# Optimization experiments

Hardware: AMD Instinct MI355X
Metric: run time of the kernel (lower is better)

Reference implementation:

```python
import jax, jax.numpy as jnp
import numpy as np

N_HEAD = 16
ROPE_CACHE = 2500  # Rotary module caches tables of length 2500
NEG_INF = -1e30


def _rope_tables(head_dim):
    inv_freq = 1.0 / (10000.0 ** (jnp.arange(0, head_dim, 2, dtype=jnp.float32) / head_dim))
    t = jnp.arange(ROPE_CACHE, dtype=jnp.float32)
    freqs = t[:, None] * inv_freq[None, :]            # (2500, head_dim//2)
    emb = jnp.concatenate([freqs, freqs], axis=-1)    # (2500, head_dim)
    return jnp.cos(emb), jnp.sin(emb)


def _rotate_half(x):
    h = x.shape[-1] // 2
    return jnp.concatenate([-x[..., h:], x[..., :h]], axis=-1)


def setup_inputs() -> dict:
    key = jax.random.key(0)
    ks = jax.random.split(key, 8)
    B, S, D = 2, 2048, 1024
    H = N_HEAD
    hd = D // H
    return {
        "qx": jax.random.normal(ks[0], (B, S, D), jnp.float32),
        "kvx": jax.random.normal(ks[1], (B, S, D), jnp.float32),
        "k_cache": jnp.zeros((B, H, S, hd), jnp.float32),
        "v_cache": jnp.zeros((B, H, S, hd), jnp.float32),
        "Wq": jax.random.normal(ks[2], (D, D), jnp.float32) * 0.02,
        "bq": jnp.zeros((D,), jnp.float32),
        "Wk": jax.random.normal(ks[3], (D, D), jnp.float32) * 0.02,
        "Wv": jax.random.normal(ks[4], (D, D), jnp.float32) * 0.02,
        "bv": jnp.zeros((D,), jnp.float32),
        "Wo": jax.random.normal(ks[5], (D, D), jnp.float32) * 0.02,
        "bo": jnp.zeros((D,), jnp.float32),
        "q_positions": jnp.arange(S, dtype=jnp.int32),
        "kv_positions": jnp.arange(S, dtype=jnp.int32),
    }


def reference(qx, kvx, k_cache, v_cache, Wq, bq, Wk, Wv, bv, Wo, bo, q_positions, kv_positions):
    B, Sq, D = qx.shape
    H = N_HEAD
    hd = D // H
    Skv = kvx.shape[1]
    cos, sin = _rope_tables(hd)
    # sqrt_qk_scale = sqrt(1) = 1, folded out.

    def rope(x, pos):  # x: (B, S, H, hd)
        c = cos[pos][None, :, None, :]
        s = sin[pos][None, :, None, :]
        return x * c + _rotate_half(x) * s

    # projections (torch Linear: y = x @ W.T + b; key has no bias)
    q = (qx @ Wq.T + bq).reshape(B, Sq, H, hd)
    q = rope(q, q_positions).transpose(0, 2, 1, 3)            # (B,H,Sq,hd)
    k = (kvx @ Wk.T).reshape(B, Skv, H, hd)
    k = rope(k, kv_positions).transpose(0, 2, 1, 3)           # (B,H,Skv,hd)
    v = (kvx @ Wv.T + bv).reshape(B, Skv, H, hd).transpose(0, 2, 1, 3)

    # KV-cache scatter update: k_cache[:, :, kv_positions] = k
    k_cache = k_cache.at[:, :, kv_positions].set(k)
    v_cache = v_cache.at[:, :, kv_positions].set(v)
    Sc = k_cache.shape[2]

    # SDPA (causal), scaled by 1/sqrt(head_dim) as in F.scaled_dot_product_attention
    scores = jnp.einsum('bhqd,bhkd->bhqk', q, k_cache) / jnp.sqrt(jnp.float32(hd))
    causal = jnp.arange(Sq)[:, None] >= jnp.arange(Sc)[None, :]
    scores = jnp.where(causal[None, None], scores, NEG_INF)
    attn = jax.nn.softmax(scores, axis=-1)
    wv = jnp.einsum('bhqk,bhkd->bhqd', attn, v_cache)

    out = wv.transpose(0, 2, 1, 3).reshape(B, Sq, D) @ Wo.T + bo
    return out
```

## Files before the change

kernel.cpp:

```cpp
#include <hip/hip_runtime.h>
#include <cstdint>
#include <cstddef>

#define NH   16
#define SEQ  2048
#define DM   1024
#define HD   64
#define KDIM 1024
#define MROWS 4096
#define CH   2

using short8  = __attribute__((ext_vector_type(8))) short;
using short4v = __attribute__((ext_vector_type(4))) short;
using floatx4 = __attribute__((ext_vector_type(4))) float;

__device__ __forceinline__ short f2bf(float f) {
  unsigned int u = __float_as_uint(f);
  u += 0x7fffu + ((u >> 16) & 1u);
  return (short)(u >> 16);
}
__device__ __forceinline__ float bf2f(short s) {
  return __uint_as_float(((unsigned int)(unsigned short)s) << 16);
}
__device__ __forceinline__ unsigned int pktrunc(float lo, float hi) {
  return __builtin_amdgcn_perm(__float_as_uint(hi), __float_as_uint(lo),
                               0x07060302u);
}

__device__ __forceinline__ void async_ld16(const void* g, void* l) {
  __builtin_amdgcn_global_load_lds(
      (const __attribute__((address_space(1))) void*)g,
      (__attribute__((address_space(3))) void*)l, 16, 0, 0);
}

struct Cvt8 {
  const float* src[8];
  void* dst[8];
  int n[8];
  const int* pos[8];
};

__global__ void convert8(Cvt8 a) {
  const int which = blockIdx.y;
  const int stride = gridDim.x * blockDim.x;
  if (which < 6) {
    const float4* s = (const float4*)a.src[which];
    short4v* d = (short4v*)a.dst[which];
    const int n4 = a.n[which] >> 2;
    for (int i = blockIdx.x * blockDim.x + threadIdx.x; i < n4; i += stride) {
      float4 v = s[i];
      short4v o;
      o.x = f2bf(v.x); o.y = f2bf(v.y); o.z = f2bf(v.z); o.w = f2bf(v.w);
      d[i] = o;
    }
  } else {
    const int* pos = a.pos[which];
    float2* d = (float2*)a.dst[which];
    const int n = a.n[which];
    for (int i = blockIdx.x * blockDim.x + threadIdx.x; i < n; i += stride) {
      int s = i >> 5, d1 = i & 31;
      float fr = __powf(10000.f, -(float)d1 * (1.f / 32.f));
      float ang = (float)pos[s] * fr;
      float sn, cs;
      __sincosf(ang, &sn, &cs);
      d[i] = make_float2(cs, sn);
    }
  }
}

__device__ __forceinline__ void gemm_core(const short* __restrict__ A,
                                          const short* __restrict__ B,
                                          int row0, int col0,
                                          short* As, short* Bs,
                                          floatx4 (&acc)[4][4], int tid) {
  const int lane = tid & 63;
  const int w = tid >> 6;
  const int quad = lane >> 4;
  const int ln = lane & 15;
  const int wr = w >> 1, wc = w & 1;

#pragma unroll
  for (int i = 0; i < 4; ++i)
#pragma unroll
    for (int j = 0; j < 4; ++j) acc[i][j] = (floatx4){0.f, 0.f, 0.f, 0.f};

  for (int k0 = 0; k0 < KDIM; k0 += 64) {
    __syncthreads();
#pragma unroll
    for (int g = 0; g < 4; ++g) {
      int slot = g * 256 + tid;
      int kk = slot >> 9, rem = slot & 511;
      int row = rem >> 2, grp = rem & 3;
      int src = k0 + kk * 32 + grp * 8;
      async_ld16(A + (size_t)(row0 + row) * KDIM + src, As + slot * 8);
      async_ld16(B + (size_t)(col0 + row) * KDIM + src, Bs + slot * 8);
    }
    __syncthreads();

#pragma unroll
    for (int ks = 0; ks < 2; ++ks) {
      short8 af[4], bfr[4];
#pragma unroll
      for (int i = 0; i < 4; ++i)
        af[i] = *(const short8*)(As + ks * 4096 + (wr * 64 + i * 16 + ln) * 32 + quad * 8);
#pragma unroll
      for (int j = 0; j < 4; ++j)
        bfr[j] = *(const short8*)(Bs + ks * 4096 + (wc * 64 + j * 16 + ln) * 32 + quad * 8);
#pragma unroll
      for (int i = 0; i < 4; ++i)
#pragma unroll
        for (int j = 0; j < 4; ++j)
          acc[i][j] = __builtin_amdgcn_mfma_f32_16x16x32_bf16(af[i], bfr[j], acc[i][j], 0, 0, 0);
    }
  }
}

__global__ __launch_bounds__(256) void proj_gemm(
    const short* __restrict__ qxb, const short* __restrict__ kvxb,
    const short* __restrict__ Wqb, const short* __restrict__ Wkb,
    const short* __restrict__ Wvb,
    const float* __restrict__ bq, const float* __restrict__ bv,
    short* __restrict__ Qo, short* __restrict__ Ko, short* __restrict__ Vt,
    const float2* __restrict__ qtab, const float2* __restrict__ ktab) {
  __shared__ __align__(16) short As[128 * 64];
  __shared__ __align__(16) short Bs[128 * 64];

  const int tid = threadIdx.x;
  const int lane = tid & 63;
  const int w = tid >> 6;
  const int quad = lane >> 4;
  const int ln = lane & 15;
  const int wr = w >> 1, wc = w & 1;
  const int z = blockIdx.z;

  int row0, col0;
  const short *A, *B;
  if (z == 2) {
    A = Wvb; B = kvxb;
    row0 = blockIdx.x * 128;
    col0 = blockIdx.y * 128;
  } else {
    A = z ? kvxb : qxb;
    B = z ? Wkb : Wqb;
    row0 = blockIdx.y * 128;
    col0 = blockIdx.x * 128;
  }

  floatx4 acc[4][4];
  gemm_core(A, B, row0, col0, As, Bs, acc, tid);

  if (z == 2) {
#pragma unroll
    for (int i = 0; i < 4; ++i)
#pragma unroll
      for (int r = 0; r < 4; ++r) {
        int nr = row0 + wr * 64 + i * 16 + quad * 4 + r;
        int h = nr >> 6, d = nr & 63;
        float bb = bv[nr];
        size_t base = ((size_t)(h)*HD + d) * SEQ;
#pragma unroll
        for (int j = 0; j < 4; ++j) {
          int sc = col0 + wc * 64 + j * 16 + ln;
          int b = sc >> 11, s = sc & (SEQ - 1);
          Vt[((size_t)b * NH * HD) * SEQ + base + s] = f2bf(acc[i][j][r] + bb);
        }
      }
  } else {
    const int colbase = col0 + wc * 64;
    const float scale = (z == 0) ? 0.125f : 1.0f;
    const float* bias = (z == 0) ? bq : nullptr;
    const float2* tab = (z == 0) ? qtab : ktab;
    short* Out = (z == 0) ? Qo : Ko;
#pragma unroll
    for (int j = 0; j < 2; ++j) {
      int col1 = colbase + j * 16 + ln;
      float b1 = bias ? bias[col1] : 0.f;
      float b2 = bias ? bias[col1 + 32] : 0.f;
      int h = col1 >> 6;
      int d1 = col1 & 63;
#pragma unroll
      for (int i = 0; i < 4; ++i)
#pragma unroll
        for (int r = 0; r < 4; ++r) {
          int row = row0 + wr * 64 + i * 16 + quad * 4 + r;
          int b = row >> 11, s = row & (SEQ - 1);
          float2 cs_sn = tab[s * 32 + d1];
          float x1 = acc[i][j][r] + b1;
          float x2 = acc[i][j + 2][r] + b2;
          float o1 = (x1 * cs_sn.x - x2 * cs_sn.y) * scale;
          float o2 = (x2 * cs_sn.x + x1 * cs_sn.y) * scale;
          size_t basq = ((((size_t)b * NH + h) * SEQ) + s) * HD;
          Out[basq + d1] = f2bf(o1);
          Out[basq + d1 + 32] = f2bf(o2);
        }
    }
  }
}

__global__ __launch_bounds__(256) void out_gemm(
    const short* __restrict__ Ab, const short* __restrict__ Bb,
    const float* __restrict__ bias, float* __restrict__ out) {
  __shared__ __align__(16) short As[64 * 64];
  __shared__ __align__(16) short Bs[128 * 64];
  const int tid = threadIdx.x;
  const int lane = tid & 63;
  const int w = tid >> 6;
  const int quad = lane >> 4;
  const int ln = lane & 15;
  const int wr = w >> 1, wc = w & 1;
  const int row0 = (blockIdx.x >> 3) * 64;
  const int col0 = (blockIdx.x & 7) * 128;

  floatx4 acc[2][4];
#pragma unroll
  for (int i = 0; i < 2; ++i)
#pragma unroll
    for (int j = 0; j < 4; ++j) acc[i][j] = (floatx4){0.f, 0.f, 0.f, 0.f};

  for (int k0 = 0; k0 < KDIM; k0 += 64) {
    __syncthreads();
    {
#pragma unroll
      for (int g = 0; g < 2; ++g) {
        int slot = g * 256 + tid;
        int kk = slot >> 8, rem = slot & 255;
        int row = rem >> 2, grp = rem & 3;
        async_ld16(Ab + (size_t)(row0 + row) * KDIM + k0 + kk * 32 + grp * 8,
                   As + slot * 8);
      }
#pragma unroll
      for (int g = 0; g < 4; ++g) {
        int slot = g * 256 + tid;
        int kk = slot >> 9, rem = slot & 511;
        int row = rem >> 2, grp = rem & 3;
        async_ld16(Bb + (size_t)(col0 + row) * KDIM + k0 + kk * 32 + grp * 8,
                   Bs + slot * 8);
      }
    }
    __syncthreads();

#pragma unroll
    for (int ks = 0; ks < 2; ++ks) {
      short8 af[2], bfr[4];
#pragma unroll
      for (int i = 0; i < 2; ++i)
        af[i] = *(const short8*)(As + ks * 2048 + (wr * 32 + i * 16 + ln) * 32 + quad * 8);
#pragma unroll
      for (int j = 0; j < 4; ++j)
        bfr[j] = *(const short8*)(Bs + ks * 4096 + (wc * 64 + j * 16 + ln) * 32 + quad * 8);
#pragma unroll
      for (int i = 0; i < 2; ++i)
#pragma unroll
        for (int j = 0; j < 4; ++j)
          acc[i][j] = __builtin_amdgcn_mfma_f32_16x16x32_bf16(af[i], bfr[j], acc[i][j], 0, 0, 0);
    }
  }

#pragma unroll
  for (int j = 0; j < 4; ++j) {
    int col = col0 + wc * 64 + j * 16 + ln;
    float bb = bias[col];
#pragma unroll
    for (int i = 0; i < 2; ++i)
#pragma unroll
      for (int r = 0; r < 4; ++r) {
        int row = row0 + wr * 32 + i * 16 + quad * 4 + r;
        out[(size_t)row * DM + col] = acc[i][j][r] + bb;
      }
  }
}

__global__ __launch_bounds__(256) void attn_partial(
    const short* __restrict__ Q, const short* __restrict__ Kc,
    const short* __restrict__ Vtg, short* __restrict__ Po,
    float* __restrict__ Lo) {
  const int tid = threadIdx.x;
  const int lane = tid & 63;
  const int w = tid >> 6;
  const int quad = lane >> 4;
  const int ln = lane & 15;
  const int bh = blockIdx.y;
  const int bx = blockIdx.x;
  const int qt = 31 - (bx >> 1);
  const int ch = bx & (CH - 1);
  if (ch > qt) return;

  const int q0 = qt * 64;
  const int wlo = q0 + w * 16;

  const short* Qb = Q + (size_t)bh * SEQ * HD;
  const short* Kb = Kc + (size_t)bh * SEQ * HD;
  const short* Vb = Vtg + (size_t)bh * HD * SEQ;

  __shared__ __align__(16) short Ks[2 * 64 * 32];
  __shared__ __align__(16) short Vs[2 * 64 * 32];
  __shared__ __align__(16) short Pt[4][16 * 72];

  short8 qa[2];
#pragma unroll
  for (int kk = 0; kk < 2; ++kk)
    qa[kk] = *(const short8*)(Qb + (size_t)(wlo + ln) * HD + quad * 8 + kk * 32);

  floatx4 oacc[4];
  float lp = 0.f;
#pragma unroll
  for (int jd = 0; jd < 4; ++jd) oacc[jd] = (floatx4){0.f, 0.f, 0.f, 0.f};

  for (int t = ch * 64; t <= q0; t += CH * 64) {
    __syncthreads();
#pragma unroll
    for (int g = 0; g < 2; ++g) {
      int slot = (w * 2 + g) * 64 + lane;
      int kk = slot >> 8, rowi = (slot >> 2) & 63, grp = slot & 3;
      async_ld16(Kb + (size_t)(t + rowi) * HD + kk * 32 + grp * 8,
                 (char*)Ks + slot * 16);
      async_ld16(Vb + (size_t)rowi * SEQ + t + kk * 32 + grp * 8,
                 (char*)Vs + slot * 16);
    }
    __syncthreads();

    floatx4 sacc[4];
#pragma unroll
    for (int c = 0; c < 4; ++c) sacc[c] = (floatx4){0.f, 0.f, 0.f, 0.f};
#pragma unroll
    for (int kk = 0; kk < 2; ++kk)
#pragma unroll
      for (int c = 0; c < 4; ++c) {
        short8 kb = *(const short8*)(Ks + kk * 2048 + (c * 16 + ln) * 32 + quad * 8);
        sacc[c] = __builtin_amdgcn_mfma_f32_16x16x32_bf16(kb, qa[kk], sacc[c], 0, 0, 0);
      }

    const bool dmask = (t == q0);
#pragma unroll
    for (int c = 0; c < 4; ++c) {
      float p[4];
#pragma unroll
      for (int r = 0; r < 4; ++r) {
        float pv = __expf(sacc[c][r]);
        if (dmask) {
          int sp = t + c * 16 + quad * 4 + r;
          int qq = wlo + ln;
          if (sp > qq) pv = 0.f;
        }
        lp += pv;
        p[r] = pv;
      }
      uint2 uu;
      uu.x = pktrunc(p[0], p[1]);
      uu.y = pktrunc(p[2], p[3]);
      *(uint2*)(&Pt[w][ln * 72 + c * 16 + quad * 4]) = uu;
    }

#pragma unroll
    for (int kk = 0; kk < 2; ++kk) {
      short8 pb = *(const short8*)(&Pt[w][ln * 72 + kk * 32 + quad * 8]);
#pragma unroll
      for (int jd = 0; jd < 4; ++jd) {
        short8 va = *(const short8*)(Vs + kk * 2048 + (jd * 16 + ln) * 32 + quad * 8);
        oacc[jd] = __builtin_amdgcn_mfma_f32_16x16x32_bf16(va, pb, oacc[jd], 0, 0, 0);
      }
    }
  }

  const size_t idx = ((size_t)bh * 32 + qt) * CH + ch;
  short* Pob = Po + idx * 4096;
#pragma unroll
  for (int jd = 0; jd < 4; ++jd) {
    short4v pk;
#pragma unroll
    for (int r = 0; r < 4; ++r) pk[r] = f2bf(oacc[jd][r]);
    *(short4v*)(Pob + (w * 16 + ln) * 64 + jd * 16 + quad * 4) = pk;
  }
  float l = lp;
  l += __shfl_xor(l, 16, 64);
  l += __shfl_xor(l, 32, 64);
  if (quad == 0) Lo[idx * 64 + w * 16 + ln] = l;
}

__global__ __launch_bounds__(256) void attn_reduce(
    const short* __restrict__ Po, const float* __restrict__ Lo,
    short* __restrict__ Ov) {
  const int qt = blockIdx.x;
  const int bh = blockIdx.y;
  const int b = bh >> 4, h = bh & 15;
  const int tid = threadIdx.x;
  const int ql = tid >> 2;
  const int d0 = (tid & 3) * 16;
  const int nch = (qt >= 1) ? CH : 1;
  const size_t i0 = ((size_t)bh * 32 + qt) * CH;

  float l = Lo[i0 * 64 + ql];
  const short8* p0 = (const short8*)(Po + i0 * 4096 + ql * 64 + d0);
  short8 a0 = p0[0], a1 = p0[1];
  float acc[16];
#pragma unroll
  for (int e = 0; e < 8; ++e) { acc[e] = bf2f(a0[e]); acc[8 + e] = bf2f(a1[e]); }
  if (nch == 2) {
    l += Lo[(i0 + 1) * 64 + ql];
    const short8* p1 = (const short8*)(Po + (i0 + 1) * 4096 + ql * 64 + d0);
    short8 c0 = p1[0], c1 = p1[1];
#pragma unroll
    for (int e = 0; e < 8; ++e) { acc[e] += bf2f(c0[e]); acc[8 + e] += bf2f(c1[e]); }
  }
  float inv = 1.f / l;
  short8 o0, o1;
#pragma unroll
  for (int e = 0; e < 8; ++e) { o0[e] = f2bf(acc[e] * inv); o1[e] = f2bf(acc[8 + e] * inv); }
  int s = qt * 64 + ql;
  short* dst = Ov + ((size_t)b * SEQ + s) * DM + h * HD + d0;
  *(short8*)dst = o0;
  *((short8*)dst + 1) = o1;
}

extern "C" void kernel_launch(void* const* d_in, const int* in_sizes, int n_in,
                              void* d_out, int out_size, void* d_ws, size_t ws_size,
                              hipStream_t stream) {
  const float* qx  = (const float*)d_in[0];
  const float* kvx = (const float*)d_in[1];
  const float* Wq = (const float*)d_in[4];
  const float* bq = (const float*)d_in[5];
  const float* Wk = (const float*)d_in[6];
  const float* Wv = (const float*)d_in[7];
  const float* bv = (const float*)d_in[8];
  const float* Wo = (const float*)d_in[9];
  const float* bo = (const float*)d_in[10];
  const int* qpos  = (const int*)d_in[11];
  const int* kvpos = (const int*)d_in[12];

  char* ws = (char*)d_ws;
  short* qxb  = (short*)(ws + 0);
  short* kvxb = (short*)(ws + 8388608);
  short* Wqb  = (short*)(ws + 16777216);
  short* Wkb  = (short*)(ws + 18874368);
  short* Wvb  = (short*)(ws + 20971520);
  short* Wob  = (short*)(ws + 23068672);
  short* Qbf  = (short*)(ws + 25165824);
  short* Kbf  = (short*)(ws + 33554432);
  short* Vtb  = (short*)(ws + 41943040);
  short* WVbf = (short*)(ws + 50331648);
  float2* qtab = (float2*)(ws + 50331648);
  float2* ktab = (float2*)(ws + 50331648 + 524288);
  short* Po = (short*)(ws + 0);
  float* Lo = (float*)(ws + 16777216);

  Cvt8 c;
  c.src[0] = qx;  c.dst[0] = qxb;  c.n[0] = MROWS * KDIM; c.pos[0] = nullptr;
  c.src[1] = kvx; c.dst[1] = kvxb; c.n[1] = MROWS * KDIM; c.pos[1] = nullptr;
  c.src[2] = Wq;  c.dst[2] = Wqb;  c.n[2] = DM * KDIM;    c.pos[2] = nullptr;
  c.src[3] = Wk;  c.dst[3] = Wkb;  c.n[3] = DM * KDIM;    c.pos[3] = nullptr;
  c.src[4] = Wv;  c.dst[4] = Wvb;  c.n[4] = DM * KDIM;    c.pos[4] = nullptr;
  c.src[5] = Wo;  c.dst[5] = Wob;  c.n[5] = DM * KDIM;    c.pos[5] = nullptr;
  c.src[6] = nullptr; c.dst[6] = qtab; c.n[6] = SEQ * 32; c.pos[6] = qpos;
  c.src[7] = nullptr; c.dst[7] = ktab; c.n[7] = SEQ * 32; c.pos[7] = kvpos;
  convert8<<<dim3(1024, 8), 256, 0, stream>>>(c);

  proj_gemm<<<dim3(DM / 128, MROWS / 128, 3), 256, 0, stream>>>(
      qxb, kvxb, Wqb, Wkb, Wvb, bq, bv, Qbf, Kbf, Vtb, qtab, ktab);

  attn_partial<<<dim3(32 * CH, 2 * NH), 256, 0, stream>>>(Qbf, Kbf, Vtb, Po, Lo);

  attn_reduce<<<dim3(SEQ / 64, 2 * NH), 256, 0, stream>>>(Po, Lo, WVbf);

  out_gemm<<<dim3(64 * 8), 256, 0, stream>>>(WVbf, Wob, bo, (float*)d_out);
}
```

Measured before the change: 256.6 us.

## Swizzle LDS tiles and double query rows per attention block

Applies an XOR swizzle to the shared-memory tile layout in both GEMMs and the attention K/V tiles, so the MFMA fragment reads avoid LDS bank conflicts. The attention partial kernel now handles 128 query rows per block, 32 per wave, instead of 64. Each K/V tile loaded into shared memory is therefore reused across twice as many queries, which halves K/V traffic and the block count. In exchange the kernel uses more registers and a larger Pt buffer, has fewer blocks for occupancy, and coarser causal tiles leave some waves idle on diagonal steps.

```diff
diff --git a/kernel.cpp b/kernel.cpp
--- a/kernel.cpp
+++ b/kernel.cpp
@@ -78,6 +78,7 @@
   const int quad = lane >> 4;
   const int ln = lane & 15;
   const int wr = w >> 1, wc = w & 1;
+  const int swz = (quad ^ ((ln >> 1) & 3)) * 8;
 
 #pragma unroll
   for (int i = 0; i < 4; ++i)
@@ -89,8 +90,9 @@
 #pragma unroll
     for (int g = 0; g < 4; ++g) {
       int slot = g * 256 + tid;
-      int kk = slot >> 9, rem = slot & 511;
-      int row = rem >> 2, grp = rem & 3;
+      int kk = slot >> 9;
+      int row = (slot >> 2) & 127;
+      int grp = (slot & 3) ^ ((slot >> 3) & 3);
       int src = k0 + kk * 32 + grp * 8;
       async_ld16(A + (size_t)(row0 + row) * KDIM + src, As + slot * 8);
       async_ld16(B + (size_t)(col0 + row) * KDIM + src, Bs + slot * 8);
@@ -102,10 +104,10 @@
       short8 af[4], bfr[4];
 #pragma unroll
       for (int i = 0; i < 4; ++i)
-        af[i] = *(const short8*)(As + ks * 4096 + (wr * 64 + i * 16 + ln) * 32 + quad * 8);
+        af[i] = *(const short8*)(As + ks * 4096 + (wr * 64 + i * 16 + ln) * 32 + swz);
 #pragma unroll
       for (int j = 0; j < 4; ++j)
-        bfr[j] = *(const short8*)(Bs + ks * 4096 + (wc * 64 + j * 16 + ln) * 32 + quad * 8);
+        bfr[j] = *(const short8*)(Bs + ks * 4096 + (wc * 64 + j * 16 + ln) * 32 + swz);
 #pragma unroll
       for (int i = 0; i < 4; ++i)
 #pragma unroll
@@ -208,6 +210,7 @@
   const int quad = lane >> 4;
   const int ln = lane & 15;
   const int wr = w >> 1, wc = w & 1;
+  const int swz = (quad ^ ((ln >> 1) & 3)) * 8;
   const int row0 = (blockIdx.x >> 3) * 64;
   const int col0 = (blockIdx.x & 7) * 128;
 
@@ -223,16 +226,18 @@
 #pragma unroll
       for (int g = 0; g < 2; ++g) {
         int slot = g * 256 + tid;
-        int kk = slot >> 8, rem = slot & 255;
-        int row = rem >> 2, grp = rem & 3;
+        int kk = slot >> 8;
+        int row = (slot >> 2) & 63;
+        int grp = (slot & 3) ^ ((slot >> 3) & 3);
         async_ld16(Ab + (size_t)(row0 + row) * KDIM + k0 + kk * 32 + grp * 8,
                    As + slot * 8);
       }
 #pragma unroll
       for (int g = 0; g < 4; ++g) {
         int slot = g * 256 + tid;
-        int kk = slot >> 9, rem = slot & 511;
-        int row = rem >> 2, grp = rem & 3;
+        int kk = slot >> 9;
+        int row = (slot >> 2) & 127;
+        int grp = (slot & 3) ^ ((slot >> 3) & 3);
         async_ld16(Bb + (size_t)(col0 + row) * KDIM + k0 + kk * 32 + grp * 8,
                    Bs + slot * 8);
       }
@@ -244,10 +249,10 @@
       short8 af[2], bfr[4];
 #pragma unroll
       for (int i = 0; i < 2; ++i)
-        af[i] = *(const short8*)(As + ks * 2048 + (wr * 32 + i * 16 + ln) * 32 + quad * 8);
+        af[i] = *(const short8*)(As + ks * 2048 + (wr * 32 + i * 16 + ln) * 32 + swz);
 #pragma unroll
       for (int j = 0; j < 4; ++j)
-        bfr[j] = *(const short8*)(Bs + ks * 4096 + (wc * 64 + j * 16 + ln) * 32 + quad * 8);
+        bfr[j] = *(const short8*)(Bs + ks * 4096 + (wc * 64 + j * 16 + ln) * 32 + swz);
 #pragma unroll
       for (int i = 0; i < 2; ++i)
 #pragma unroll
@@ -279,14 +284,14 @@
   const int w = tid >> 6;
   const int quad = lane >> 4;
   const int ln = lane & 15;
+  const int swz = (quad ^ ((ln >> 1) & 3)) * 8;
   const int bh = blockIdx.y;
   const int bx = blockIdx.x;
-  const int qt = 31 - (bx >> 1);
-  const int ch = bx & (CH - 1);
-  if (ch > qt) return;
-
-  const int q0 = qt * 64;
-  const int wlo = q0 + w * 16;
+  const int QT = 15 - (bx >> 1);
+  const int ch = bx & 1;
+
+  const int q0 = QT * 128;
+  const int wlo = q0 + w * 32;
 
   const short* Qb = Q + (size_t)bh * SEQ * HD;
   const short* Kb = Kc + (size_t)bh * SEQ * HD;
@@ -294,24 +299,33 @@
 
   __shared__ __align__(16) short Ks[2 * 64 * 32];
   __shared__ __align__(16) short Vs[2 * 64 * 32];
-  __shared__ __align__(16) short Pt[4][16 * 72];
-
-  short8 qa[2];
-#pragma unroll
-  for (int kk = 0; kk < 2; ++kk)
-    qa[kk] = *(const short8*)(Qb + (size_t)(wlo + ln) * HD + quad * 8 + kk * 32);
-
-  floatx4 oacc[4];
-  float lp = 0.f;
-#pragma unroll
-  for (int jd = 0; jd < 4; ++jd) oacc[jd] = (floatx4){0.f, 0.f, 0.f, 0.f};
-
-  for (int t = ch * 64; t <= q0; t += CH * 64) {
+  __shared__ __align__(16) short Pt[4][32 * 72];
+
+  short8 qa[2][2];
+#pragma unroll
+  for (int i = 0; i < 2; ++i)
+#pragma unroll
+    for (int kk = 0; kk < 2; ++kk)
+      qa[i][kk] = *(const short8*)(Qb + (size_t)(wlo + i * 16 + ln) * HD +
+                                   quad * 8 + kk * 32);
+
+  floatx4 oacc[4][2];
+  float lp[2];
+#pragma unroll
+  for (int jd = 0; jd < 4; ++jd)
+#pragma unroll
+    for (int i = 0; i < 2; ++i) oacc[jd][i] = (floatx4){0.f, 0.f, 0.f, 0.f};
+  lp[0] = lp[1] = 0.f;
+
+  const int t_end = q0 + 128;
+  for (int t = ch * 64; t < t_end; t += CH * 64) {
     __syncthreads();
 #pragma unroll
     for (int g = 0; g < 2; ++g) {
       int slot = (w * 2 + g) * 64 + lane;
-      int kk = slot >> 8, rowi = (slot >> 2) & 63, grp = slot & 3;
+      int kk = slot >> 8;
+      int rowi = (slot >> 2) & 63;
+      int grp = (slot & 3) ^ ((slot >> 3) & 3);
       async_ld16(Kb + (size_t)(t + rowi) * HD + kk * 32 + grp * 8,
                  (char*)Ks + slot * 16);
       async_ld16(Vb + (size_t)rowi * SEQ + t + kk * 32 + grp * 8,
@@ -319,94 +333,100 @@
     }
     __syncthreads();
 
-    floatx4 sacc[4];
-#pragma unroll
-    for (int c = 0; c < 4; ++c) sacc[c] = (floatx4){0.f, 0.f, 0.f, 0.f};
+    if (t > wlo + 31) continue;
+
+    floatx4 sacc[4][2];
+#pragma unroll
+    for (int c = 0; c < 4; ++c)
+#pragma unroll
+      for (int i = 0; i < 2; ++i) sacc[c][i] = (floatx4){0.f, 0.f, 0.f, 0.f};
 #pragma unroll
     for (int kk = 0; kk < 2; ++kk)
 #pragma unroll
       for (int c = 0; c < 4; ++c) {
-        short8 kb = *(const short8*)(Ks + kk * 2048 + (c * 16 + ln) * 32 + quad * 8);
-        sacc[c] = __builtin_amdgcn_mfma_f32_16x16x32_bf16(kb, qa[kk], sacc[c], 0, 0, 0);
-      }
-
-    const bool dmask = (t == q0);
-#pragma unroll
-    for (int c = 0; c < 4; ++c) {
-      float p[4];
-#pragma unroll
-      for (int r = 0; r < 4; ++r) {
-        float pv = __expf(sacc[c][r]);
-        if (dmask) {
-          int sp = t + c * 16 + quad * 4 + r;
-          int qq = wlo + ln;
-          if (sp > qq) pv = 0.f;
+        short8 kb = *(const short8*)(Ks + kk * 2048 + (c * 16 + ln) * 32 + swz);
+        sacc[c][0] = __builtin_amdgcn_mfma_f32_16x16x32_bf16(kb, qa[0][kk], sacc[c][0], 0, 0, 0);
+        sacc[c][1] = __builtin_amdgcn_mfma_f32_16x16x32_bf16(kb, qa[1][kk], sacc[c][1], 0, 0, 0);
+      }
+
+    const bool dmask = (t + 63 > wlo);
+#pragma unroll
+    for (int c = 0; c < 4; ++c)
+#pragma unroll
+      for (int i = 0; i < 2; ++i) {
+        float p[4];
+#pragma unroll
+        for (int r = 0; r < 4; ++r) {
+          float pv = __expf(sacc[c][i][r]);
+          if (dmask) {
+            int sp = t + c * 16 + quad * 4 + r;
+            int qq = wlo + i * 16 + ln;
+            if (sp > qq) pv = 0.f;
+          }
+          lp[i] += pv;
+          p[r] = pv;
         }
-        lp += pv;
-        p[r] = pv;
-      }
-      uint2 uu;
-      uu.x = pktrunc(p[0], p[1]);
-      uu.y = pktrunc(p[2], p[3]);
-      *(uint2*)(&Pt[w][ln * 72 + c * 16 + quad * 4]) = uu;
-    }
+        uint2 uu;
+        uu.x = pktrunc(p[0], p[1]);
+        uu.y = pktrunc(p[2], p[3]);
+        *(uint2*)(&Pt[w][(i * 16 + ln) * 72 + c * 16 + quad * 4]) = uu;
+      }
 
 #pragma unroll
     for (int kk = 0; kk < 2; ++kk) {
-      short8 pb = *(const short8*)(&Pt[w][ln * 72 + kk * 32 + quad * 8]);
+      short8 pb0 = *(const short8*)(&Pt[w][(ln) * 72 + kk * 32 + quad * 8]);
+      short8 pb1 = *(const short8*)(&Pt[w][(16 + ln) * 72 + kk * 32 + quad * 8]);
 #pragma unroll
       for (int jd = 0; jd < 4; ++jd) {
-        short8 va = *(const short8*)(Vs + kk * 2048 + (jd * 16 + ln) * 32 + quad * 8);
-        oacc[jd] = __builtin_amdgcn_mfma_f32_16x16x32_bf16(va, pb, oacc[jd], 0, 0, 0);
-      }
-    }
-  }
-
-  const size_t idx = ((size_t)bh * 32 + qt) * CH + ch;
-  short* Pob = Po + idx * 4096;
-#pragma unroll
-  for (int jd = 0; jd < 4; ++jd) {
-    short4v pk;
-#pragma unroll
-    for (int r = 0; r < 4; ++r) pk[r] = f2bf(oacc[jd][r]);
-    *(short4v*)(Pob + (w * 16 + ln) * 64 + jd * 16 + quad * 4) = pk;
-  }
-  float l = lp;
-  l += __shfl_xor(l, 16, 64);
-  l += __shfl_xor(l, 32, 64);
-  if (quad == 0) Lo[idx * 64 + w * 16 + ln] = l;
+        short8 va = *(const short8*)(Vs + kk * 2048 + (jd * 16 + ln) * 32 + swz);
+        oacc[jd][0] = __builtin_amdgcn_mfma_f32_16x16x32_bf16(va, pb0, oacc[jd][0], 0, 0, 0);
+        oacc[jd][1] = __builtin_amdgcn_mfma_f32_16x16x32_bf16(va, pb1, oacc[jd][1], 0, 0, 0);
+      }
+    }
+  }
+
+  const size_t idx = ((size_t)bh * 16 + QT) * CH + ch;
+  short* Pob = Po + idx * 8192;
+#pragma unroll
+  for (int jd = 0; jd < 4; ++jd)
+#pragma unroll
+    for (int i = 0; i < 2; ++i) {
+      short4v pk;
+#pragma unroll
+      for (int r = 0; r < 4; ++r) pk[r] = f2bf(oacc[jd][i][r]);
+      *(short4v*)(Pob + (w * 32 + i * 16 + ln) * 64 + jd * 16 + quad * 4) = pk;
+    }
+#pragma unroll
+  for (int i = 0; i < 2; ++i) {
+    float l = lp[i];
+    l += __shfl_xor(l, 16, 64);
+    l += __shfl_xor(l, 32, 64);
+    if (quad == 0) Lo[idx * 128 + w * 32 + i * 16 + ln] = l;
+  }
 }
 
 __global__ __launch_bounds__(256) void attn_reduce(
     const short* __restrict__ Po, const float* __restrict__ Lo,
     short* __restrict__ Ov) {
-  const int qt = blockIdx.x;
   const int bh = blockIdx.y;
   const int b = bh >> 4, h = bh & 15;
   const int tid = threadIdx.x;
-  const int ql = tid >> 2;
+  const int s = blockIdx.x * 64 + (tid >> 2);
   const int d0 = (tid & 3) * 16;
-  const int nch = (qt >= 1) ? CH : 1;
-  const size_t i0 = ((size_t)bh * 32 + qt) * CH;
-
-  float l = Lo[i0 * 64 + ql];
-  const short8* p0 = (const short8*)(Po + i0 * 4096 + ql * 64 + d0);
-  short8 a0 = p0[0], a1 = p0[1];
-  float acc[16];
-#pragma unroll
-  for (int e = 0; e < 8; ++e) { acc[e] = bf2f(a0[e]); acc[8 + e] = bf2f(a1[e]); }
-  if (nch == 2) {
-    l += Lo[(i0 + 1) * 64 + ql];
-    const short8* p1 = (const short8*)(Po + (i0 + 1) * 4096 + ql * 64 + d0);
-    short8 c0 = p1[0], c1 = p1[1];
-#pragma unroll
-    for (int e = 0; e < 8; ++e) { acc[e] += bf2f(c0[e]); acc[8 + e] += bf2f(c1[e]); }
-  }
+  const int QT = s >> 7, ql = s & 127;
+  const size_t i0 = ((size_t)bh * 16 + QT) * CH;
+
+  float l = Lo[i0 * 128 + ql] + Lo[(i0 + 1) * 128 + ql];
+  const short8* p0 = (const short8*)(Po + i0 * 8192 + ql * 64 + d0);
+  const short8* p1 = (const short8*)(Po + (i0 + 1) * 8192 + ql * 64 + d0);
+  short8 a0 = p0[0], a1 = p0[1], c0 = p1[0], c1 = p1[1];
   float inv = 1.f / l;
   short8 o0, o1;
 #pragma unroll
-  for (int e = 0; e < 8; ++e) { o0[e] = f2bf(acc[e] * inv); o1[e] = f2bf(acc[8 + e] * inv); }
-  int s = qt * 64 + ql;
+  for (int e = 0; e < 8; ++e) {
+    o0[e] = f2bf((bf2f(a0[e]) + bf2f(c0[e])) * inv);
+    o1[e] = f2bf((bf2f(a1[e]) + bf2f(c1[e])) * inv);
+  }
   short* dst = Ov + ((size_t)b * SEQ + s) * DM + h * HD + d0;
   *(short8*)dst = o0;
   *((short8*)dst + 1) = o1;
@@ -457,7 +477,7 @@
   proj_gemm<<<dim3(DM / 128, MROWS / 128, 3), 256, 0, stream>>>(
       qxb, kvxb, Wqb, Wkb, Wvb, bq, bv, Qbf, Kbf, Vtb, qtab, ktab);
 
-  attn_partial<<<dim3(32 * CH, 2 * NH), 256, 0, stream>>>(Qbf, Kbf, Vtb, Po, Lo);
+  attn_partial<<<dim3(16 * CH, 2 * NH), 256, 0, stream>>>(Qbf, Kbf, Vtb, Po, Lo);
 
   attn_reduce<<<dim3(SEQ / 64, 2 * NH), 256, 0, stream>>>(Po, Lo, WVbf);
 
```

Result: no change. 261.3 us (+1.8%).

## Fuse attention split-reduce into output GEMM and XOR-swizzle LDS tiles

Applied to the files above, without the earlier changes.

Removes the separate attn_reduce kernel. The output GEMM now loads both partial attention chunks, sums them, normalizes by the combined row sums, converts to bf16 and writes the A tile into shared memory directly. Empty chunks are zero-filled in attn_partial so the reduction needs no branch. Shared-memory tiles in all GEMM and attention kernels also get an XOR swizzle on the 16-byte group index to cut LDS bank conflicts. This saves one launch and one round trip through global memory, but the A operand now goes through synchronous loads and conversion inside the GEMM k-loop. Each output-GEMM column block also repeats the reduction work.

```diff
diff --git a/kernel.cpp b/kernel.cpp
--- a/kernel.cpp
+++ b/kernel.cpp
@@ -78,6 +78,7 @@
   const int quad = lane >> 4;
   const int ln = lane & 15;
   const int wr = w >> 1, wc = w & 1;
+  const int swz = (quad ^ ((ln >> 1) & 3)) * 8;
 
 #pragma unroll
   for (int i = 0; i < 4; ++i)
@@ -89,8 +90,9 @@
 #pragma unroll
     for (int g = 0; g < 4; ++g) {
       int slot = g * 256 + tid;
-      int kk = slot >> 9, rem = slot & 511;
-      int row = rem >> 2, grp = rem & 3;
+      int kk = slot >> 9;
+      int row = (slot >> 2) & 127;
+      int grp = (slot & 3) ^ ((slot >> 3) & 3);
       int src = k0 + kk * 32 + grp * 8;
       async_ld16(A + (size_t)(row0 + row) * KDIM + src, As + slot * 8);
       async_ld16(B + (size_t)(col0 + row) * KDIM + src, Bs + slot * 8);
@@ -102,10 +104,10 @@
       short8 af[4], bfr[4];
 #pragma unroll
       for (int i = 0; i < 4; ++i)
-        af[i] = *(const short8*)(As + ks * 4096 + (wr * 64 + i * 16 + ln) * 32 + quad * 8);
+        af[i] = *(const short8*)(As + ks * 4096 + (wr * 64 + i * 16 + ln) * 32 + swz);
 #pragma unroll
       for (int j = 0; j < 4; ++j)
-        bfr[j] = *(const short8*)(Bs + ks * 4096 + (wc * 64 + j * 16 + ln) * 32 + quad * 8);
+        bfr[j] = *(const short8*)(Bs + ks * 4096 + (wc * 64 + j * 16 + ln) * 32 + swz);
 #pragma unroll
       for (int i = 0; i < 4; ++i)
 #pragma unroll
@@ -198,7 +200,8 @@
 }
 
 __global__ __launch_bounds__(256) void out_gemm(
-    const short* __restrict__ Ab, const short* __restrict__ Bb,
+    const short* __restrict__ Po, const float* __restrict__ Lo,
+    const short* __restrict__ Bb,
     const float* __restrict__ bias, float* __restrict__ out) {
   __shared__ __align__(16) short As[64 * 64];
   __shared__ __align__(16) short Bs[128 * 64];
@@ -208,8 +211,11 @@
   const int quad = lane >> 4;
   const int ln = lane & 15;
   const int wr = w >> 1, wc = w & 1;
+  const int swz = (quad ^ ((ln >> 1) & 3)) * 8;
   const int row0 = (blockIdx.x >> 3) * 64;
   const int col0 = (blockIdx.x & 7) * 128;
+  const int b16 = (row0 >> 11) * 16;
+  const int qt = (row0 & (SEQ - 1)) >> 6;
 
   floatx4 acc[2][4];
 #pragma unroll
@@ -220,19 +226,38 @@
   for (int k0 = 0; k0 < KDIM; k0 += 64) {
     __syncthreads();
     {
+      const int h = k0 >> 6;
+      const size_t ib = ((size_t)(b16 + h) * 32 + qt) * CH;
+      const short* P0 = Po + (ib + 0) * 4096;
+      const short* P1 = Po + (ib + 1) * 4096;
+      const float* L0 = Lo + (ib + 0) * 64;
+      const float* L1 = Lo + (ib + 1) * 64;
 #pragma unroll
       for (int g = 0; g < 2; ++g) {
         int slot = g * 256 + tid;
-        int kk = slot >> 8, rem = slot & 255;
-        int row = rem >> 2, grp = rem & 3;
-        async_ld16(Ab + (size_t)(row0 + row) * KDIM + k0 + kk * 32 + grp * 8,
-                   As + slot * 8);
+        int kk = slot >> 8;
+        int row = (slot >> 2) & 63;
+        int grp = (slot & 3) ^ ((slot >> 3) & 3);
+        int off = row * 64 + kk * 32 + grp * 8;
+        short8 a0 = *(const short8*)(P0 + off);
+        short8 a1 = *(const short8*)(P1 + off);
+        float inv = 1.f / (L0[row] + L1[row]);
+        float v[8];
+#pragma unroll
+        for (int e = 0; e < 8; ++e) v[e] = (bf2f(a0[e]) + bf2f(a1[e])) * inv;
+        uint4 u;
+        u.x = pktrunc(v[0], v[1]);
+        u.y = pktrunc(v[2], v[3]);
+        u.z = pktrunc(v[4], v[5]);
+        u.w = pktrunc(v[6], v[7]);
+        *(uint4*)(As + slot * 8) = u;
       }
 #pragma unroll
       for (int g = 0; g < 4; ++g) {
         int slot = g * 256 + tid;
-        int kk = slot >> 9, rem = slot & 511;
-        int row = rem >> 2, grp = rem & 3;
+        int kk = slot >> 9;
+        int row = (slot >> 2) & 127;
+        int grp = (slot & 3) ^ ((slot >> 3) & 3);
         async_ld16(Bb + (size_t)(col0 + row) * KDIM + k0 + kk * 32 + grp * 8,
                    Bs + slot * 8);
       }
@@ -244,10 +269,10 @@
       short8 af[2], bfr[4];
 #pragma unroll
       for (int i = 0; i < 2; ++i)
-        af[i] = *(const short8*)(As + ks * 2048 + (wr * 32 + i * 16 + ln) * 32 + quad * 8);
+        af[i] = *(const short8*)(As + ks * 2048 + (wr * 32 + i * 16 + ln) * 32 + swz);
 #pragma unroll
       for (int j = 0; j < 4; ++j)
-        bfr[j] = *(const short8*)(Bs + ks * 4096 + (wc * 64 + j * 16 + ln) * 32 + quad * 8);
+        bfr[j] = *(const short8*)(Bs + ks * 4096 + (wc * 64 + j * 16 + ln) * 32 + swz);
 #pragma unroll
       for (int i = 0; i < 2; ++i)
 #pragma unroll
@@ -279,11 +304,21 @@
   const int w = tid >> 6;
   const int quad = lane >> 4;
   const int ln = lane & 15;
+  const int swz = (quad ^ ((ln >> 1) & 3)) * 8;
   const int bh = blockIdx.y;
   const int bx = blockIdx.x;
   const int qt = 31 - (bx >> 1);
   const int ch = bx & (CH - 1);
-  if (ch > qt) return;
+  const size_t idx = ((size_t)bh * 32 + qt) * CH + ch;
+
+  if (ch > qt) {
+    short8 z = (short8){0, 0, 0, 0, 0, 0, 0, 0};
+    short8* Pz = (short8*)(Po + idx * 4096);
+    Pz[tid] = z;
+    Pz[256 + tid] = z;
+    if (tid < 64) Lo[idx * 64 + tid] = 0.f;
+    return;
+  }
 
   const int q0 = qt * 64;
   const int wlo = q0 + w * 16;
@@ -311,7 +346,9 @@
 #pragma unroll
     for (int g = 0; g < 2; ++g) {
       int slot = (w * 2 + g) * 64 + lane;
-      int kk = slot >> 8, rowi = (slot >> 2) & 63, grp = slot & 3;
+      int kk = slot >> 8;
+      int rowi = (slot >> 2) & 63;
+      int grp = (slot & 3) ^ ((slot >> 3) & 3);
       async_ld16(Kb + (size_t)(t + rowi) * HD + kk * 32 + grp * 8,
                  (char*)Ks + slot * 16);
       async_ld16(Vb + (size_t)rowi * SEQ + t + kk * 32 + grp * 8,
@@ -326,7 +363,7 @@
     for (int kk = 0; kk < 2; ++kk)
 #pragma unroll
       for (int c = 0; c < 4; ++c) {
-        short8 kb = *(const short8*)(Ks + kk * 2048 + (c * 16 + ln) * 32 + quad * 8);
+        short8 kb = *(const short8*)(Ks + kk * 2048 + (c * 16 + ln) * 32 + swz);
         sacc[c] = __builtin_amdgcn_mfma_f32_16x16x32_bf16(kb, qa[kk], sacc[c], 0, 0, 0);
       }
 
@@ -356,13 +393,12 @@
       short8 pb = *(const short8*)(&Pt[w][ln * 72 + kk * 32 + quad * 8]);
 #pragma unroll
       for (int jd = 0; jd < 4; ++jd) {
-        short8 va = *(const short8*)(Vs + kk * 2048 + (jd * 16 + ln) * 32 + quad * 8);
+        short8 va = *(const short8*)(Vs + kk * 2048 + (jd * 16 + ln) * 32 + swz);
         oacc[jd] = __builtin_amdgcn_mfma_f32_16x16x32_bf16(va, pb, oacc[jd], 0, 0, 0);
       }
     }
   }
 
-  const size_t idx = ((size_t)bh * 32 + qt) * CH + ch;
   short* Pob = Po + idx * 4096;
 #pragma unroll
   for (int jd = 0; jd < 4; ++jd) {
@@ -375,41 +411,6 @@
   l += __shfl_xor(l, 16, 64);
   l += __shfl_xor(l, 32, 64);
   if (quad == 0) Lo[idx * 64 + w * 16 + ln] = l;
-}
-
-__global__ __launch_bounds__(256) void attn_reduce(
-    const short* __restrict__ Po, const float* __restrict__ Lo,
-    short* __restrict__ Ov) {
-  const int qt = blockIdx.x;
-  const int bh = blockIdx.y;
-  const int b = bh >> 4, h = bh & 15;
-  const int tid = threadIdx.x;
-  const int ql = tid >> 2;
-  const int d0 = (tid & 3) * 16;
-  const int nch = (qt >= 1) ? CH : 1;
-  const size_t i0 = ((size_t)bh * 32 + qt) * CH;
-
-  float l = Lo[i0 * 64 + ql];
-  const short8* p0 = (const short8*)(Po + i0 * 4096 + ql * 64 + d0);
-  short8 a0 = p0[0], a1 = p0[1];
-  float acc[16];
-#pragma unroll
-  for (int e = 0; e < 8; ++e) { acc[e] = bf2f(a0[e]); acc[8 + e] = bf2f(a1[e]); }
-  if (nch == 2) {
-    l += Lo[(i0 + 1) * 64 + ql];
-    const short8* p1 = (const short8*)(Po + (i0 + 1) * 4096 + ql * 64 + d0);
-    short8 c0 = p1[0], c1 = p1[1];
-#pragma unroll
-    for (int e = 0; e < 8; ++e) { acc[e] += bf2f(c0[e]); acc[8 + e] += bf2f(c1[e]); }
-  }
-  float inv = 1.f / l;
-  short8 o0, o1;
-#pragma unroll
-  for (int e = 0; e < 8; ++e) { o0[e] = f2bf(acc[e] * inv); o1[e] = f2bf(acc[8 + e] * inv); }
-  int s = qt * 64 + ql;
-  short* dst = Ov + ((size_t)b * SEQ + s) * DM + h * HD + d0;
-  *(short8*)dst = o0;
-  *((short8*)dst + 1) = o1;
 }
 
 extern "C" void kernel_launch(void* const* d_in, const int* in_sizes, int n_in,
@@ -437,7 +438,6 @@
   short* Qbf  = (short*)(ws + 25165824);
   short* Kbf  = (short*)(ws + 33554432);
   short* Vtb  = (short*)(ws + 41943040);
-  short* WVbf = (short*)(ws + 50331648);
   float2* qtab = (float2*)(ws + 50331648);
   float2* ktab = (float2*)(ws + 50331648 + 524288);
   short* Po = (short*)(ws + 0);
@@ -459,7 +459,5 @@
 
   attn_partial<<<dim3(32 * CH, 2 * NH), 256, 0, stream>>>(Qbf, Kbf, Vtb, Po, Lo);
 
-  attn_reduce<<<dim3(SEQ / 64, 2 * NH), 256, 0, stream>>>(Po, Lo, WVbf);
-
-  out_gemm<<<dim3(64 * 8), 256, 0, stream>>>(WVbf, Wob, bo, (float*)d_out);
-}
+  out_gemm<<<dim3(64 * 8), 256, 0, stream>>>(Po, Lo, Wob, bo, (float*)d_out);
+}
```

Measured after the change: 253.4 us. No clear change (-1.2%).
